# Optimization experiments

Hardware: AMD Instinct MI355X
Metric: run time of the kernel (lower is better)

## Reference

```python
import jax, jax.numpy as jnp
import numpy as np
from jax import lax

B, S, DIM, H, D = 8, 256, 64, 2, 100
TEMP = 10.0
EPS = 1e-5

def _conv(x, W, b):
    # Conv2d with kernel (H,1), VALID padding, NCHW layout
    y = lax.conv_general_dilated(x, W, (1, 1), 'VALID',
                                 dimension_numbers=('NCHW', 'OIHW', 'NCHW'))
    return y + b[None, :, None, None]

def _bn(x, g, b, m, v):
    # BatchNorm2d in inference mode (running stats)
    scale = (g / jnp.sqrt(v + EPS))[None, :, None, None]
    return (x - m[None, :, None, None]) * scale + b[None, :, None, None]

def setup_inputs() -> dict:
    key = jax.random.key(0)
    ks = jax.random.split(key, 12)
    p = lambda k, sh, s=0.05: jax.random.normal(k, sh, jnp.float32) * s
    return {
        'q': jax.random.normal(ks[0], (B, S, DIM), jnp.float32),
        'k': jax.random.normal(ks[1], (B, S, DIM), jnp.float32),
        'v': jax.random.normal(ks[2], (B, S, DIM), jnp.float32),
        'W1': p(ks[3], (D, 2 * DIM, H, 1)), 'b1': p(ks[4], (D,)),
        'g1': jnp.ones((D,), jnp.float32), 'be1': jnp.zeros((D,), jnp.float32),
        'm1': p(ks[5], (D,)), 'var1': jnp.ones((D,), jnp.float32),
        'W2': p(ks[6], (D, D, H, 1)), 'b2': p(ks[7], (D,)),
        'g2': jnp.ones((D,), jnp.float32), 'be2': jnp.zeros((D,), jnp.float32),
        'm2': p(ks[8], (D,)), 'var2': jnp.ones((D,), jnp.float32),
        'W3': p(ks[9], (1, D, H, 1)), 'b3': p(ks[10], (1,)),
    }

def reference(q, k, v, W1, b1, g1, be1, m1, var1, W2, b2, g2, be2, m2, var2, W3, b3):
    Bq, Sq, T = q.shape
    # q -> (B,T,S,1) broadcast over keys; k -> (B,T,1,S) broadcast over queries
    qe = jnp.broadcast_to(q.transpose(0, 2, 1)[:, :, :, None], (Bq, T, Sq, Sq))
    ke = jnp.broadcast_to(k.transpose(0, 2, 1)[:, :, None, :], (Bq, T, Sq, Sq))
    a = jnp.concatenate([qe, ke], axis=1)            # (B, 2T, S, S)
    a = _conv(a, W1, b1)                             # (B, D, S-H+1, S)
    res = a
    a = jnp.pad(a, ((0, 0), (0, 0), (H - 1, 0), (0, 0)))  # pad height back to S
    a = _bn(a, g1, be1, m1, var1)
    a = _conv(jax.nn.relu(a), W2, b2)                # (B, D, S-H+1, S)
    a = _bn(a + res, g2, be2, m2, var2)
    a = _conv(jax.nn.relu(a), W3, b3)                # (B, 1, S-2H+2, S)
    a = a[:, 0] / TEMP                               # (B, S-2H+2, S)
    attn = jax.nn.softmax(a, axis=2)
    out = jnp.matmul(attn, v)                        # (B, S-2H+2, T)
    return out, attn
```

## Files before the change

kernel.cpp:

```cpp
#include <hip/hip_runtime.h>
#include <hip/hip_bf16.h>

typedef float floatx4 __attribute__((ext_vector_type(4)));
typedef short bhalf8  __attribute__((ext_vector_type(8)));
typedef unsigned short ush;
typedef unsigned int uint;

#define EPS 1e-5f

constexpr int Bb = 8, S = 256, T = 64, Dc = 100;
constexpr int SH = 255;
constexpr int SO = 254;
constexpr int CK = 128;
constexpr int CR = 112;
constexpr int LSTR = 136;

constexpr size_t OFF_U1   = 0;
constexpr size_t OFF_S2   = 512;
constexpr size_t OFF_W30  = 1024;
constexpr size_t OFF_W31  = 1536;
constexpr size_t OFF_W1T  = 2048;
constexpr size_t OFF_W1KT = OFF_W1T + 65536;
constexpr size_t OFF_W2P  = OFF_W1KT + 32768;
constexpr size_t OFF_AQS  = OFF_W2P + 57344;
constexpr size_t OFF_AQE  = OFF_AQS + (size_t)Bb*SH*CK*4;
constexpr size_t OFF_AKF  = OFF_AQE + (size_t)Bb*SH*CK*4;
constexpr size_t OFF_AKEF = OFF_AKF + (size_t)Bb*16*4*64*8*4;
constexpr size_t OFF_Z0   = OFF_AKEF + (size_t)Bb*16*7*64*4*4;
constexpr size_t OFF_Z1   = OFF_Z0 + (size_t)Bb*SH*S*4;

__device__ __forceinline__ uint pkbf(float lo, float hi) {
    uint a = __float_as_uint(lo) + 0x8000u;
    uint b = __float_as_uint(hi) + 0x8000u;
    return __builtin_amdgcn_perm(b, a, 0x07060302u);
}

__global__ __launch_bounds__(128) void k_prep0(const float* __restrict__ W1, const float* __restrict__ W2,
                                               const float* __restrict__ g1, const float* __restrict__ be1,
                                               const float* __restrict__ m1, const float* __restrict__ var1,
                                               const float* __restrict__ g2, const float* __restrict__ var2,
                                               const float* __restrict__ W3,
                                               float* __restrict__ W1T, float* __restrict__ W1kT,
                                               ush* __restrict__ W2p,
                                               float* __restrict__ U1, float* __restrict__ S2,
                                               float* __restrict__ W30, float* __restrict__ W31) {
    const int bid = blockIdx.x, tid = threadIdx.x;
    if (bid < 128) {
        int k = bid, c = tid;
        W1T[k * 128 + c] = (c < Dc) ? W1[(size_t)c * 256 + k] : 0.f;
    } else if (bid < 192) {
        int t = bid - 128, c = tid;
        W1kT[t * 128 + c] = (c < Dc) ? (W1[(size_t)c * 256 + 128 + 2 * t] + W1[(size_t)c * 256 + 129 + 2 * t]) : 0.f;
    } else if (bid < 416) {
        int idx = (bid - 192) * 128 + tid;
        int h = idx / (CR * CK);
        int rem = idx % (CR * CK);
        int c = rem / CK, cp = rem % CK;
        float v = (c < Dc && cp < Dc) ? W2[((size_t)c * Dc + cp) * 2 + h] : 0.f;
        __hip_bfloat16 bv = __float2bfloat16(v);
        W2p[idx] = *reinterpret_cast<ush*>(&bv);
    } else {
        int c = tid;
        float u1 = 0.f, s2 = 0.f, w0 = 0.f, w1 = 0.f;
        if (c < Dc) {
            float sg1 = g1[c] / sqrtf(var1[c] + EPS);
            u1 = be1[c] - m1[c] * sg1;
            s2 = g2[c] / sqrtf(var2[c] + EPS);
            w0 = W3[c * 2 + 0];
            w1 = W3[c * 2 + 1];
        }
        U1[c] = u1; S2[c] = s2; W30[c] = w0; W31[c] = w1;
    }
}

__global__ __launch_bounds__(128) void k_prep1(const float* __restrict__ q, const float* __restrict__ kin,
                                               const float* __restrict__ b1,
                                               const float* __restrict__ W1T, const float* __restrict__ W1kT,
                                               const float* __restrict__ g1, const float* __restrict__ be1,
                                               const float* __restrict__ m1, const float* __restrict__ var1,
                                               const float* __restrict__ g2, const float* __restrict__ be2,
                                               const float* __restrict__ m2, const float* __restrict__ var2,
                                               const float* __restrict__ b2,
                                               float* __restrict__ AqS, float* __restrict__ AqE,
                                               float* __restrict__ AkF, float* __restrict__ AkEF) {
    __shared__ float xs[5 * 64];
    const int bid = blockIdx.x;
    const int b = blockIdx.y;
    const int c = threadIdx.x;
    float s1 = 0.f, u1 = 0.f, s2 = 0.f, u2 = 0.f;
    if (c < Dc) {
        s1 = g1[c] / sqrtf(var1[c] + EPS);
        u1 = be1[c] - m1[c] * s1;
        s2 = g2[c] / sqrtf(var2[c] + EPS);
        u2 = (b2[c] - m2[c]) * s2 + be2[c];
    }
    if (bid < 64) {
        const int i0 = bid * 4;
        const int nr = (i0 + 4 <= SH) ? 4 : (SH - i0);
        for (int idx = c; idx < (nr + 1) * 64; idx += 128)
            xs[idx] = q[((size_t)b * S + i0 + (idx >> 6)) * T + (idx & 63)];
        __syncthreads();
        float acc[4] = {0.f, 0.f, 0.f, 0.f};
        const float* wt = W1T + c;
        #pragma unroll 4
        for (int k = 0; k < 128; ++k) {
            const float w = wt[(size_t)k * 128];
            const int t = k >> 1, h = k & 1;
            #pragma unroll
            for (int r = 0; r < 4; ++r)
                acc[r] = fmaf(xs[(r + h) * 64 + t], w, acc[r]);
        }
        const float b1v = (c < Dc) ? b1[c] : 0.f;
        for (int r = 0; r < nr; ++r) {
            float s = (c < Dc) ? (acc[r] + b1v) : 0.f;
            size_t row = ((size_t)b * SH + i0 + r) * CK + c;
            AqS[row] = s * s1 + u1;
            AqE[row] = s * s2 + u2;
        }
    } else {
        const int j0 = (bid - 64) * 4;
        for (int idx = c; idx < 4 * 64; idx += 128)
            xs[idx] = kin[((size_t)b * S + j0 + (idx >> 6)) * T + (idx & 63)];
        __syncthreads();
        float acc[4] = {0.f, 0.f, 0.f, 0.f};
        const float* wt = W1kT + c;
        #pragma unroll 4
        for (int t = 0; t < 64; ++t) {
            const float w = wt[(size_t)t * 128];
            #pragma unroll
            for (int r = 0; r < 4; ++r)
                acc[r] = fmaf(xs[r * 64 + t], w, acc[r]);
        }
        const int ks = c >> 5, qq = (c >> 3) & 3, e = c & 7;
        const int ct = c >> 4, q2 = (c >> 2) & 3, rr = c & 3;
        #pragma unroll
        for (int r = 0; r < 4; ++r) {
            const int j = j0 + r;
            const int j16 = j >> 4, ln = j & 15;
            const float s = (c < Dc) ? acc[r] : 0.f;
            AkF[((((size_t)b * 16 + j16) * 4 + ks) * 64 + qq * 16 + ln) * 8 + e] = s * s1;
            if (c < 112)
                AkEF[((((size_t)b * 16 + j16) * 7 + ct) * 64 + q2 * 16 + ln) * 4 + rr] = s * s2;
        }
    }
}

__global__ __launch_bounds__(512, 4) void k_main(const float* __restrict__ AqS, const float* __restrict__ AqE,
                                                 const float* __restrict__ AkF, const float* __restrict__ AkEF,
                                                 const ush* __restrict__ W2p,
                                                 const float* __restrict__ U1, const float* __restrict__ S2,
                                                 const float* __restrict__ W30f, const float* __restrict__ W31f,
                                                 float* __restrict__ Z0, float* __restrict__ Z1) {
    __shared__ __align__(16) ush W2s[2 * CR * LSTR];
    const int tid = threadIdx.x;
    const int wv = tid >> 6, lane = tid & 63, ln = lane & 15, quad = lane >> 4;
    const int ip = blockIdx.x, b = blockIdx.y;
    const int j16A = wv << 1;

    floatx4 acc0[7], acc1[7];
    #pragma unroll
    for (int ct = 0; ct < 7; ++ct) {
        acc0[ct] = (floatx4){0.f, 0.f, 0.f, 0.f};
        acc1[ct] = (floatx4){0.f, 0.f, 0.f, 0.f};
    }

    for (int idx = tid; idx < 2 * CR * 16; idx += 512) {
        int row = idx >> 4, ch = idx & 15;
        *reinterpret_cast<uint4*>(&W2s[row * LSTR + ch * 8]) =
            *reinterpret_cast<const uint4*>(&W2p[row * CK + ch * 8]);
    }
    __syncthreads();

    const float* fA = AkF + ((size_t)(b * 16 + j16A) * 4 * 64 + lane) * 8;
    const float* fB = fA + 4 * 64 * 8;
    const float* aq0 = (ip == 0) ? U1 : (AqS + (size_t)(b * SH + ip - 1) * CK);
    const float* aq1 = AqS + (size_t)(b * SH + ip) * CK;
    const bool pad0 = (ip == 0);

    #pragma unroll 1
    for (int ks = 0; ks < 4; ++ks) {
        const int k0 = ks * 32 + quad * 8;
        const float4 ka = *reinterpret_cast<const float4*>(fA + ks * 512);
        const float4 kb = *reinterpret_cast<const float4*>(fA + ks * 512 + 4);
        const float4 kc = *reinterpret_cast<const float4*>(fB + ks * 512);
        const float4 kd = *reinterpret_cast<const float4*>(fB + ks * 512 + 4);
        {
            const float4 qa = *reinterpret_cast<const float4*>(aq0 + k0);
            const float4 qb = *reinterpret_cast<const float4*>(aq0 + k0 + 4);
            uint4 p, rr;
            if (pad0) {
                p.x = pkbf(fmaxf(qa.x, 0.f), fmaxf(qa.y, 0.f));
                p.y = pkbf(fmaxf(qa.z, 0.f), fmaxf(qa.w, 0.f));
                p.z = pkbf(fmaxf(qb.x, 0.f), fmaxf(qb.y, 0.f));
                p.w = pkbf(fmaxf(qb.z, 0.f), fmaxf(qb.w, 0.f));
                rr = p;
            } else {
                p.x  = pkbf(fmaxf(qa.x + ka.x, 0.f), fmaxf(qa.y + ka.y, 0.f));
                p.y  = pkbf(fmaxf(qa.z + ka.z, 0.f), fmaxf(qa.w + ka.w, 0.f));
                p.z  = pkbf(fmaxf(qb.x + kb.x, 0.f), fmaxf(qb.y + kb.y, 0.f));
                p.w  = pkbf(fmaxf(qb.z + kb.z, 0.f), fmaxf(qb.w + kb.w, 0.f));
                rr.x = pkbf(fmaxf(qa.x + kc.x, 0.f), fmaxf(qa.y + kc.y, 0.f));
                rr.y = pkbf(fmaxf(qa.z + kc.z, 0.f), fmaxf(qa.w + kc.w, 0.f));
                rr.z = pkbf(fmaxf(qb.x + kd.x, 0.f), fmaxf(qb.y + kd.y, 0.f));
                rr.w = pkbf(fmaxf(qb.z + kd.z, 0.f), fmaxf(qb.w + kd.w, 0.f));
            }
            const bhalf8 bf0 = *reinterpret_cast<bhalf8*>(&p);
            const bhalf8 bf1 = *reinterpret_cast<bhalf8*>(&rr);
            #pragma unroll
            for (int ct = 0; ct < 7; ++ct) {
                const bhalf8 af = *reinterpret_cast<const bhalf8*>(&W2s[(ct * 16 + ln) * LSTR + k0]);
                acc0[ct] = __builtin_amdgcn_mfma_f32_16x16x32_bf16(af, bf0, acc0[ct], 0, 0, 0);
                acc1[ct] = __builtin_amdgcn_mfma_f32_16x16x32_bf16(af, bf1, acc1[ct], 0, 0, 0);
            }
        }
        {
            const float4 qa = *reinterpret_cast<const float4*>(aq1 + k0);
            const float4 qb = *reinterpret_cast<const float4*>(aq1 + k0 + 4);
            uint4 p, rr;
            p.x  = pkbf(fmaxf(qa.x + ka.x, 0.f), fmaxf(qa.y + ka.y, 0.f));
            p.y  = pkbf(fmaxf(qa.z + ka.z, 0.f), fmaxf(qa.w + ka.w, 0.f));
            p.z  = pkbf(fmaxf(qb.x + kb.x, 0.f), fmaxf(qb.y + kb.y, 0.f));
            p.w  = pkbf(fmaxf(qb.z + kb.z, 0.f), fmaxf(qb.w + kb.w, 0.f));
            rr.x = pkbf(fmaxf(qa.x + kc.x, 0.f), fmaxf(qa.y + kc.y, 0.f));
            rr.y = pkbf(fmaxf(qa.z + kc.z, 0.f), fmaxf(qa.w + kc.w, 0.f));
            rr.z = pkbf(fmaxf(qb.x + kd.x, 0.f), fmaxf(qb.y + kd.y, 0.f));
            rr.w = pkbf(fmaxf(qb.z + kd.z, 0.f), fmaxf(qb.w + kd.w, 0.f));
            const bhalf8 bf0 = *reinterpret_cast<bhalf8*>(&p);
            const bhalf8 bf1 = *reinterpret_cast<bhalf8*>(&rr);
            #pragma unroll
            for (int ct = 0; ct < 7; ++ct) {
                const bhalf8 af = *reinterpret_cast<const bhalf8*>(&W2s[(CR + ct * 16 + ln) * LSTR + k0]);
                acc0[ct] = __builtin_amdgcn_mfma_f32_16x16x32_bf16(af, bf0, acc0[ct], 0, 0, 0);
                acc1[ct] = __builtin_amdgcn_mfma_f32_16x16x32_bf16(af, bf1, acc1[ct], 0, 0, 0);
            }
        }
    }

    float z0a = 0.f, z1a = 0.f, z0b = 0.f, z1b = 0.f;
    const float* aqer = AqE + (size_t)(b * SH + ip) * CK;
    const float* eA = AkEF + ((size_t)(b * 16 + j16A) * 7 * 64 + lane) * 4;
    const float* eB = eA + 7 * 64 * 4;
    #pragma unroll
    for (int ct = 0; ct < 7; ++ct) {
        const int c = ct * 16 + (quad << 2);
        const float4 aq  = *reinterpret_cast<const float4*>(aqer + c);
        const float4 aka = *reinterpret_cast<const float4*>(eA + ct * 256);
        const float4 akb = *reinterpret_cast<const float4*>(eB + ct * 256);
        const float4 s2  = *reinterpret_cast<const float4*>(S2 + c);
        const float4 w0  = *reinterpret_cast<const float4*>(W30f + c);
        const float4 w1  = *reinterpret_cast<const float4*>(W31f + c);
        const float aqv[4] = {aq.x, aq.y, aq.z, aq.w};
        const float kav[4] = {aka.x, aka.y, aka.z, aka.w};
        const float kbv[4] = {akb.x, akb.y, akb.z, akb.w};
        const float s2v[4] = {s2.x, s2.y, s2.z, s2.w};
        const float w0v[4] = {w0.x, w0.y, w0.z, w0.w};
        const float w1v[4] = {w1.x, w1.y, w1.z, w1.w};
        #pragma unroll
        for (int r = 0; r < 4; ++r) {
            float ta = fmaxf(fmaf(acc0[ct][r], s2v[r], aqv[r] + kav[r]), 0.f);
            z0a = fmaf(ta, w0v[r], z0a);
            z1a = fmaf(ta, w1v[r], z1a);
            float tb = fmaxf(fmaf(acc1[ct][r], s2v[r], aqv[r] + kbv[r]), 0.f);
            z0b = fmaf(tb, w0v[r], z0b);
            z1b = fmaf(tb, w1v[r], z1b);
        }
    }
    z0a += __shfl_xor(z0a, 16, 64); z0a += __shfl_xor(z0a, 32, 64);
    z1a += __shfl_xor(z1a, 16, 64); z1a += __shfl_xor(z1a, 32, 64);
    z0b += __shfl_xor(z0b, 16, 64); z0b += __shfl_xor(z0b, 32, 64);
    z1b += __shfl_xor(z1b, 16, 64); z1b += __shfl_xor(z1b, 32, 64);
    if (lane < 16) {
        size_t zi = (size_t)(b * SH + ip) * S + wv * 32 + lane;
        Z0[zi] = z0a; Z1[zi] = z1a;
        Z0[zi + 16] = z0b; Z1[zi + 16] = z1b;
    }
}

__global__ __launch_bounds__(256) void k_soft(const float* __restrict__ Z0, const float* __restrict__ Z1,
                                              const float* __restrict__ v,
                                              const float* __restrict__ b3,
                                              float* __restrict__ outp,
                                              float* __restrict__ attnp) {
    __shared__ float attn_s[4][256];
    const int wv = threadIdx.x >> 6, lane = threadIdx.x & 63;
    const int i = blockIdx.x * 4 + wv;
    const int b = blockIdx.y;
    if (i >= SO) return;
    const float b3f = b3[0];
    const size_t zr = (size_t)(b * SH + i) * S;
    const float4 z0 = *reinterpret_cast<const float4*>(Z0 + zr + lane * 4);
    const float4 z1 = *reinterpret_cast<const float4*>(Z1 + zr + S + lane * 4);
    float l0 = (z0.x + z1.x + b3f) * 0.1f;
    float l1 = (z0.y + z1.y + b3f) * 0.1f;
    float l2 = (z0.z + z1.z + b3f) * 0.1f;
    float l3 = (z0.w + z1.w + b3f) * 0.1f;

    float mx = fmaxf(fmaxf(l0, l1), fmaxf(l2, l3));
    #pragma unroll
    for (int o = 1; o < 64; o <<= 1) mx = fmaxf(mx, __shfl_xor(mx, o, 64));
    float e0 = __expf(l0 - mx), e1 = __expf(l1 - mx), e2 = __expf(l2 - mx), e3 = __expf(l3 - mx);
    float sm = e0 + e1 + e2 + e3;
    #pragma unroll
    for (int o = 1; o < 64; o <<= 1) sm += __shfl_xor(sm, o, 64);
    const float inv = 1.f / sm;
    const float a0 = e0 * inv, a1 = e1 * inv, a2 = e2 * inv, a3 = e3 * inv;
    *reinterpret_cast<float4*>(attnp + (size_t)(b * SO + i) * S + lane * 4) = make_float4(a0, a1, a2, a3);
    *reinterpret_cast<float4*>(&attn_s[wv][lane * 4]) = make_float4(a0, a1, a2, a3);

    const float* vb = v + (size_t)b * S * T + lane;
    float p0 = 0.f, p1 = 0.f, p2 = 0.f, p3 = 0.f;
    #pragma unroll 4
    for (int j = 0; j < 256; j += 4) {
        p0 = fmaf(attn_s[wv][j],     vb[(size_t)j * T],       p0);
        p1 = fmaf(attn_s[wv][j + 1], vb[(size_t)(j + 1) * T], p1);
        p2 = fmaf(attn_s[wv][j + 2], vb[(size_t)(j + 2) * T], p2);
        p3 = fmaf(attn_s[wv][j + 3], vb[(size_t)(j + 3) * T], p3);
    }
    outp[(size_t)(b * SO + i) * T + lane] = (p0 + p1) + (p2 + p3);
}

extern "C" void kernel_launch(void* const* d_in, const int* in_sizes, int n_in,
                              void* d_out, int out_size, void* d_ws, size_t ws_size,
                              hipStream_t stream) {
    const float* q    = (const float*)d_in[0];
    const float* kin  = (const float*)d_in[1];
    const float* vin  = (const float*)d_in[2];
    const float* W1   = (const float*)d_in[3];
    const float* b1   = (const float*)d_in[4];
    const float* g1   = (const float*)d_in[5];
    const float* be1  = (const float*)d_in[6];
    const float* m1   = (const float*)d_in[7];
    const float* var1 = (const float*)d_in[8];
    const float* W2   = (const float*)d_in[9];
    const float* b2   = (const float*)d_in[10];
    const float* g2   = (const float*)d_in[11];
    const float* be2  = (const float*)d_in[12];
    const float* m2   = (const float*)d_in[13];
    const float* var2 = (const float*)d_in[14];
    const float* W3   = (const float*)d_in[15];
    const float* b3   = (const float*)d_in[16];

    char* ws = (char*)d_ws;
    float* U1   = (float*)(ws + OFF_U1);
    float* S2p  = (float*)(ws + OFF_S2);
    float* W30  = (float*)(ws + OFF_W30);
    float* W31  = (float*)(ws + OFF_W31);
    float* W1T  = (float*)(ws + OFF_W1T);
    float* W1kT = (float*)(ws + OFF_W1KT);
    ush*   W2p  = (ush*)(ws + OFF_W2P);
    float* AqS  = (float*)(ws + OFF_AQS);
    float* AqE  = (float*)(ws + OFF_AQE);
    float* AkF  = (float*)(ws + OFF_AKF);
    float* AkEF = (float*)(ws + OFF_AKEF);
    float* Z0   = (float*)(ws + OFF_Z0);
    float* Z1   = (float*)(ws + OFF_Z1);

    float* outp  = (float*)d_out;
    float* attnp = outp + (size_t)Bb * SO * T;

    k_prep0<<<417, 128, 0, stream>>>(W1, W2, g1, be1, m1, var1, g2, var2, W3,
                                     W1T, W1kT, W2p, U1, S2p, W30, W31);
    k_prep1<<<dim3(128, Bb), 128, 0, stream>>>(q, kin, b1, W1T, W1kT,
                                               g1, be1, m1, var1, g2, be2, m2, var2, b2,
                                               AqS, AqE, AkF, AkEF);
    k_main<<<dim3(SH, Bb), 512, 0, stream>>>(AqS, AqE, AkF, AkEF, W2p, U1, S2p, W30, W31, Z0, Z1);
    k_soft<<<dim3((SO + 3) / 4, Bb), 256, 0, stream>>>(Z0, Z1, vin, b3, outp, attnp);
}
```

Before: 168.3 us.

## Merge weight prep and projection kernels, staging W1 in shared memory

Folds the two preparation kernels into one launch. Each projection block now loads W1 (or the summed key half of W1) straight into padded shared memory instead of reading a pre-transposed global copy, and handles 8 rows rather than 4. This drops one kernel launch, the intermediate transposed weight buffers and the dependency between the two prep stages. The cost is that every block reloads about 50KB of weights into LDS, which adds redundant global traffic and lowers occupancy from the large shared allocation.

```diff
diff --git a/kernel.cpp b/kernel.cpp
--- a/kernel.cpp
+++ b/kernel.cpp
@@ -19,9 +19,7 @@
 constexpr size_t OFF_S2   = 512;
 constexpr size_t OFF_W30  = 1024;
 constexpr size_t OFF_W31  = 1536;
-constexpr size_t OFF_W1T  = 2048;
-constexpr size_t OFF_W1KT = OFF_W1T + 65536;
-constexpr size_t OFF_W2P  = OFF_W1KT + 32768;
+constexpr size_t OFF_W2P  = 2048;
 constexpr size_t OFF_AQS  = OFF_W2P + 57344;
 constexpr size_t OFF_AQE  = OFF_AQS + (size_t)Bb*SH*CK*4;
 constexpr size_t OFF_AKF  = OFF_AQE + (size_t)Bb*SH*CK*4;
@@ -29,64 +27,57 @@
 constexpr size_t OFF_Z0   = OFF_AKEF + (size_t)Bb*16*7*64*4*4;
 constexpr size_t OFF_Z1   = OFF_Z0 + (size_t)Bb*SH*S*4;
 
+constexpr int NAQT = 256;
+constexpr int NAKT = 256;
+constexpr int NW2  = 224;
+
 __device__ __forceinline__ uint pkbf(float lo, float hi) {
     uint a = __float_as_uint(lo) + 0x8000u;
     uint b = __float_as_uint(hi) + 0x8000u;
     return __builtin_amdgcn_perm(b, a, 0x07060302u);
 }
 
-__global__ __launch_bounds__(128) void k_prep0(const float* __restrict__ W1, const float* __restrict__ W2,
-                                               const float* __restrict__ g1, const float* __restrict__ be1,
-                                               const float* __restrict__ m1, const float* __restrict__ var1,
-                                               const float* __restrict__ g2, const float* __restrict__ var2,
-                                               const float* __restrict__ W3,
-                                               float* __restrict__ W1T, float* __restrict__ W1kT,
-                                               ush* __restrict__ W2p,
-                                               float* __restrict__ U1, float* __restrict__ S2,
-                                               float* __restrict__ W30, float* __restrict__ W31) {
-    const int bid = blockIdx.x, tid = threadIdx.x;
-    if (bid < 128) {
-        int k = bid, c = tid;
-        W1T[k * 128 + c] = (c < Dc) ? W1[(size_t)c * 256 + k] : 0.f;
-    } else if (bid < 192) {
-        int t = bid - 128, c = tid;
-        W1kT[t * 128 + c] = (c < Dc) ? (W1[(size_t)c * 256 + 128 + 2 * t] + W1[(size_t)c * 256 + 129 + 2 * t]) : 0.f;
-    } else if (bid < 416) {
-        int idx = (bid - 192) * 128 + tid;
-        int h = idx / (CR * CK);
-        int rem = idx % (CR * CK);
-        int c = rem / CK, cp = rem % CK;
-        float v = (c < Dc && cp < Dc) ? W2[((size_t)c * Dc + cp) * 2 + h] : 0.f;
-        __hip_bfloat16 bv = __float2bfloat16(v);
-        W2p[idx] = *reinterpret_cast<ush*>(&bv);
-    } else {
-        int c = tid;
-        float u1 = 0.f, s2 = 0.f, w0 = 0.f, w1 = 0.f;
-        if (c < Dc) {
-            float sg1 = g1[c] / sqrtf(var1[c] + EPS);
-            u1 = be1[c] - m1[c] * sg1;
-            s2 = g2[c] / sqrtf(var2[c] + EPS);
-            w0 = W3[c * 2 + 0];
-            w1 = W3[c * 2 + 1];
-        }
-        U1[c] = u1; S2[c] = s2; W30[c] = w0; W31[c] = w1;
-    }
-}
-
-__global__ __launch_bounds__(128) void k_prep1(const float* __restrict__ q, const float* __restrict__ kin,
-                                               const float* __restrict__ b1,
-                                               const float* __restrict__ W1T, const float* __restrict__ W1kT,
-                                               const float* __restrict__ g1, const float* __restrict__ be1,
-                                               const float* __restrict__ m1, const float* __restrict__ var1,
-                                               const float* __restrict__ g2, const float* __restrict__ be2,
-                                               const float* __restrict__ m2, const float* __restrict__ var2,
-                                               const float* __restrict__ b2,
-                                               float* __restrict__ AqS, float* __restrict__ AqE,
-                                               float* __restrict__ AkF, float* __restrict__ AkEF) {
-    __shared__ float xs[5 * 64];
-    const int bid = blockIdx.x;
-    const int b = blockIdx.y;
-    const int c = threadIdx.x;
+__global__ __launch_bounds__(128) void k_prep(const float* __restrict__ q, const float* __restrict__ kin,
+                                              const float* __restrict__ W1, const float* __restrict__ b1,
+                                              const float* __restrict__ g1, const float* __restrict__ be1,
+                                              const float* __restrict__ m1, const float* __restrict__ var1,
+                                              const float* __restrict__ W2, const float* __restrict__ b2,
+                                              const float* __restrict__ g2, const float* __restrict__ be2,
+                                              const float* __restrict__ m2, const float* __restrict__ var2,
+                                              const float* __restrict__ W3,
+                                              ush* __restrict__ W2p,
+                                              float* __restrict__ U1, float* __restrict__ S2,
+                                              float* __restrict__ W30, float* __restrict__ W31,
+                                              float* __restrict__ AqS, float* __restrict__ AqE,
+                                              float* __restrict__ AkF, float* __restrict__ AkEF) {
+    __shared__ float sh[100 * 129 + 9 * 64];
+    float* xs = sh + 100 * 129;
+    const int bid = blockIdx.x, c = threadIdx.x;
+
+    if (bid >= NAQT + NAKT) {
+        int r = bid - NAQT - NAKT;
+        if (r < NW2) {
+            int idx = r * 128 + c;
+            int h = idx / (CR * CK);
+            int rem = idx % (CR * CK);
+            int cc = rem / CK, cp = rem % CK;
+            float v = (cc < Dc && cp < Dc) ? W2[((size_t)cc * Dc + cp) * 2 + h] : 0.f;
+            __hip_bfloat16 bv = __float2bfloat16(v);
+            W2p[idx] = *reinterpret_cast<ush*>(&bv);
+        } else {
+            float u1 = 0.f, s2 = 0.f, w0 = 0.f, w1 = 0.f;
+            if (c < Dc) {
+                float sg1 = g1[c] / sqrtf(var1[c] + EPS);
+                u1 = be1[c] - m1[c] * sg1;
+                s2 = g2[c] / sqrtf(var2[c] + EPS);
+                w0 = W3[c * 2 + 0];
+                w1 = W3[c * 2 + 1];
+            }
+            U1[c] = u1; S2[c] = s2; W30[c] = w0; W31[c] = w1;
+        }
+        return;
+    }
+
     float s1 = 0.f, u1 = 0.f, s2 = 0.f, u2 = 0.f;
     if (c < Dc) {
         s1 = g1[c] / sqrtf(var1[c] + EPS);
@@ -94,21 +85,28 @@
         s2 = g2[c] / sqrtf(var2[c] + EPS);
         u2 = (b2[c] - m2[c]) * s2 + be2[c];
     }
-    if (bid < 64) {
-        const int i0 = bid * 4;
-        const int nr = (i0 + 4 <= SH) ? 4 : (SH - i0);
+
+    if (bid < NAQT) {
+        const int tile = bid & 31, b = bid >> 5;
+        const int i0 = tile * 8;
+        const int nr = (i0 + 8 <= SH) ? 8 : (SH - i0);
+        for (int idx = c; idx < 100 * 128; idx += 128) {
+            int cc = idx >> 7, k = idx & 127;
+            sh[cc * 129 + k] = W1[(size_t)cc * 256 + k];
+        }
         for (int idx = c; idx < (nr + 1) * 64; idx += 128)
             xs[idx] = q[((size_t)b * S + i0 + (idx >> 6)) * T + (idx & 63)];
         __syncthreads();
-        float acc[4] = {0.f, 0.f, 0.f, 0.f};
-        const float* wt = W1T + c;
-        #pragma unroll 4
-        for (int k = 0; k < 128; ++k) {
-            const float w = wt[(size_t)k * 128];
-            const int t = k >> 1, h = k & 1;
-            #pragma unroll
-            for (int r = 0; r < 4; ++r)
-                acc[r] = fmaf(xs[(r + h) * 64 + t], w, acc[r]);
+        float acc[8] = {0.f, 0.f, 0.f, 0.f, 0.f, 0.f, 0.f, 0.f};
+        if (c < Dc) {
+            const float* wr = sh + c * 129;
+            #pragma unroll 2
+            for (int t = 0; t < 64; ++t) {
+                const float w0 = wr[2 * t], w1 = wr[2 * t + 1];
+                #pragma unroll
+                for (int r = 0; r < 8; ++r)
+                    acc[r] = fmaf(xs[r * 64 + t], w0, fmaf(xs[(r + 1) * 64 + t], w1, acc[r]));
+            }
         }
         const float b1v = (c < Dc) ? b1[c] : 0.f;
         for (int r = 0; r < nr; ++r) {
@@ -118,29 +116,38 @@
             AqE[row] = s * s2 + u2;
         }
     } else {
-        const int j0 = (bid - 64) * 4;
-        for (int idx = c; idx < 4 * 64; idx += 128)
+        const int r0 = bid - NAQT;
+        const int tile = r0 & 31, b = r0 >> 5;
+        const int j0 = tile * 8;
+        for (int idx = c; idx < 100 * 64; idx += 128) {
+            int cc = idx >> 6, t = idx & 63;
+            const float2 p = reinterpret_cast<const float2*>(W1 + (size_t)cc * 256 + 128)[t];
+            sh[cc * 129 + t] = p.x + p.y;
+        }
+        for (int idx = c; idx < 8 * 64; idx += 128)
             xs[idx] = kin[((size_t)b * S + j0 + (idx >> 6)) * T + (idx & 63)];
         __syncthreads();
-        float acc[4] = {0.f, 0.f, 0.f, 0.f};
-        const float* wt = W1kT + c;
-        #pragma unroll 4
-        for (int t = 0; t < 64; ++t) {
-            const float w = wt[(size_t)t * 128];
-            #pragma unroll
-            for (int r = 0; r < 4; ++r)
-                acc[r] = fmaf(xs[r * 64 + t], w, acc[r]);
+        float acc[8] = {0.f, 0.f, 0.f, 0.f, 0.f, 0.f, 0.f, 0.f};
+        if (c < Dc) {
+            const float* wr = sh + c * 129;
+            #pragma unroll 2
+            for (int t = 0; t < 64; ++t) {
+                const float w = wr[t];
+                #pragma unroll
+                for (int r = 0; r < 8; ++r)
+                    acc[r] = fmaf(xs[r * 64 + t], w, acc[r]);
+            }
         }
         const int ks = c >> 5, qq = (c >> 3) & 3, e = c & 7;
-        const int ct = c >> 4, q2 = (c >> 2) & 3, rr = c & 3;
+        const int ct = c >> 4, q2 = (c >> 2) & 3, rr2 = c & 3;
         #pragma unroll
-        for (int r = 0; r < 4; ++r) {
+        for (int r = 0; r < 8; ++r) {
             const int j = j0 + r;
             const int j16 = j >> 4, ln = j & 15;
             const float s = (c < Dc) ? acc[r] : 0.f;
             AkF[((((size_t)b * 16 + j16) * 4 + ks) * 64 + qq * 16 + ln) * 8 + e] = s * s1;
             if (c < 112)
-                AkEF[((((size_t)b * 16 + j16) * 7 + ct) * 64 + q2 * 16 + ln) * 4 + rr] = s * s2;
+                AkEF[((((size_t)b * 16 + j16) * 7 + ct) * 64 + q2 * 16 + ln) * 4 + rr2] = s * s2;
         }
     }
 }
@@ -345,8 +352,6 @@
     float* S2p  = (float*)(ws + OFF_S2);
     float* W30  = (float*)(ws + OFF_W30);
     float* W31  = (float*)(ws + OFF_W31);
-    float* W1T  = (float*)(ws + OFF_W1T);
-    float* W1kT = (float*)(ws + OFF_W1KT);
     ush*   W2p  = (ush*)(ws + OFF_W2P);
     float* AqS  = (float*)(ws + OFF_AQS);
     float* AqE  = (float*)(ws + OFF_AQE);
@@ -358,11 +363,10 @@
     float* outp  = (float*)d_out;
     float* attnp = outp + (size_t)Bb * SO * T;
 
-    k_prep0<<<417, 128, 0, stream>>>(W1, W2, g1, be1, m1, var1, g2, var2, W3,
-                                     W1T, W1kT, W2p, U1, S2p, W30, W31);
-    k_prep1<<<dim3(128, Bb), 128, 0, stream>>>(q, kin, b1, W1T, W1kT,
-                                               g1, be1, m1, var1, g2, be2, m2, var2, b2,
-                                               AqS, AqE, AkF, AkEF);
+    k_prep<<<NAQT + NAKT + NW2 + 1, 128, 0, stream>>>(q, kin, W1, b1, g1, be1, m1, var1,
+                                                      W2, b2, g2, be2, m2, var2, W3,
+                                                      W2p, U1, S2p, W30, W31,
+                                                      AqS, AqE, AkF, AkEF);
     k_main<<<dim3(SH, Bb), 512, 0, stream>>>(AqS, AqE, AkF, AkEF, W2p, U1, S2p, W30, W31, Z0, Z1);
     k_soft<<<dim3((SO + 3) / 4, Bb), 256, 0, stream>>>(Z0, Z1, vin, b3, outp, attnp);
 }
```

Measured after the change: 168.8 us. No clear change (+0.3%).
